# Kernel tuning notes

Measured on AMD Instinct MI355X. Metric: run time of the kernel, lower is better.

Reference implementation:

```python
import jax, jax.numpy as jnp
import numpy as np

IN_CH = 256
OUT_CH = 256
NUM_HEADS = 4
LOCAL_RADIUS = 2
SCALE = OUT_CH ** 0.5  # torch divides by out_channels**0.5


def setup_inputs() -> dict:
    key = jax.random.key(0)
    ks = jax.random.split(key, 7)
    B, C, H, W = 1, IN_CH, 48, 48
    x = jax.random.normal(ks[0], (B, C, H, W), dtype=jnp.float32)
    s = 0.02
    Wq = jax.random.normal(ks[1], (OUT_CH, IN_CH), dtype=jnp.float32) * s
    Wk = jax.random.normal(ks[2], (OUT_CH, IN_CH), dtype=jnp.float32) * s
    Wv = jax.random.normal(ks[3], (OUT_CH, IN_CH), dtype=jnp.float32) * s
    bq = jax.random.normal(ks[4], (OUT_CH,), dtype=jnp.float32) * s
    bk = jax.random.normal(ks[5], (OUT_CH,), dtype=jnp.float32) * s
    bv = jax.random.normal(ks[6], (OUT_CH,), dtype=jnp.float32) * s
    return {"x": x, "Wq": Wq, "bq": bq, "Wk": Wk, "bk": bk, "Wv": Wv, "bv": bv}


def reference(x, Wq, bq, Wk, bk, Wv, bv):
    B, C, H, W = x.shape
    N = H * W
    # Faithful to torch: x.view(B, N, -1) is a raw reshape of [B,C,H,W]
    xr = x.reshape(B, N, C)
    q = xr @ Wq.T + bq  # [B, N, OUT_CH]
    k = xr @ Wk.T + bk
    v = xr @ Wv.T + bv
    dh = OUT_CH // NUM_HEADS
    # [B, heads, N, dh]
    q = q.reshape(B, N, NUM_HEADS, dh).transpose(0, 2, 1, 3)
    k = k.reshape(B, N, NUM_HEADS, dh).transpose(0, 2, 1, 3)
    v = v.reshape(B, N, NUM_HEADS, dh).transpose(0, 2, 1, 3)
    acc = jnp.zeros_like(v)
    for h in range(-LOCAL_RADIUS, LOCAL_RADIUS + 1):
        for w in range(-LOCAL_RADIUS, LOCAL_RADIUS + 1):
            # torch rolls dims (-3, -2) of [B, heads, N, dh] -> axes (1, 2)
            rk = jnp.roll(k, shift=(h, w), axis=(1, 2))
            scores = jnp.einsum('bhnd,bhmd->bhnm', q, rk) / SCALE
            p = jax.nn.softmax(scores, axis=-1)  # dropout p=0 -> identity
            rv = jnp.roll(v, shift=(-h, -w), axis=(1, 2))
            acc = acc + jnp.einsum('bhnm,bhmd->bhnd', p, rv)
    out = acc.transpose(0, 2, 1, 3).reshape(B, N, NUM_HEADS * dh)
    return out
```

## Files before the change

kernel.cpp:

```cpp
#include <hip/hip_runtime.h>


#define N_TOK 2304
#define OUTC 256
#define HSZ (N_TOK * 64)

typedef _Float16 half8 __attribute__((ext_vector_type(8)));
typedef _Float16 half4 __attribute__((ext_vector_type(4)));
typedef float f32x4 __attribute__((ext_vector_type(4)));

__device__ __forceinline__ f32x4 mfma16(half8 a, half8 b, f32x4 c) {
  return __builtin_amdgcn_mfma_f32_16x16x32_f16(a, b, c, 0, 0, 0);
}

__global__ __launch_bounds__(256) void k_convert(
    const float* __restrict__ x, const float* __restrict__ Wq,
    const float* __restrict__ Wk, const float* __restrict__ Wv,
    _Float16* __restrict__ xh, _Float16* __restrict__ Wh) {
  int i = blockIdx.x * 256 + threadIdx.x;
  if (i < N_TOK * OUTC / 4) {
    float4 f = ((const float4*)x)[i];
    half4 h; h[0] = (_Float16)f.x; h[1] = (_Float16)f.y; h[2] = (_Float16)f.z; h[3] = (_Float16)f.w;
    ((half4*)xh)[i] = h;
  }
  if (i < OUTC * OUTC / 4) {
    float4 a = ((const float4*)Wq)[i];
    float4 b = ((const float4*)Wk)[i];
    float4 c = ((const float4*)Wv)[i];
    half4 ha, hb, hc;
    ha[0]=(_Float16)a.x; ha[1]=(_Float16)a.y; ha[2]=(_Float16)a.z; ha[3]=(_Float16)a.w;
    hb[0]=(_Float16)b.x; hb[1]=(_Float16)b.y; hb[2]=(_Float16)b.z; hb[3]=(_Float16)b.w;
    hc[0]=(_Float16)c.x; hc[1]=(_Float16)c.y; hc[2]=(_Float16)c.z; hc[3]=(_Float16)c.w;
    ((half4*)Wh)[i] = ha;
    ((half4*)(Wh + OUTC*OUTC))[i] = hb;
    ((half4*)(Wh + 2*OUTC*OUTC))[i] = hc;
  }
}

__global__ __launch_bounds__(256) void k_proj(
    const _Float16* __restrict__ xh, const _Float16* __restrict__ Wh,
    const float* __restrict__ bq, const float* __restrict__ bk,
    const float* __restrict__ bv,
    _Float16* __restrict__ Qh, _Float16* __restrict__ KF, float* __restrict__ VfT) {
  const int w = threadIdx.x >> 6, lane = threadIdx.x & 63;
  const int lr = lane & 15, lk = lane >> 4;
  const int n0 = blockIdx.x * 64 + w * 16;
  const int o0 = blockIdx.y * 64;
  const int mat = blockIdx.z;
  const _Float16* W = Wh + mat * (OUTC * OUTC);
  f32x4 acc[4] = {};
  const _Float16* xrow = xh + (n0 + lr) * OUTC + 8 * lk;
#pragma unroll
  for (int kk = 0; kk < 8; ++kk) {
    half8 a = *(const half8*)(xrow + 32 * kk);
#pragma unroll
    for (int c = 0; c < 4; ++c) {
      half8 b = *(const half8*)(W + (o0 + 16*c + lr) * OUTC + 32*kk + 8*lk);
      acc[c] = mfma16(a, b, acc[c]);
    }
  }
  const float* bias = (mat == 0) ? bq : (mat == 1) ? bk : bv;
  const int hd = blockIdx.y;
#pragma unroll
  for (int c = 0; c < 4; ++c) {
    int o = o0 + 16*c + lr;
    float bo = bias[o];
    if (mat == 2) {
      float4 vv;
      vv.x = acc[c][0] + bo; vv.y = acc[c][1] + bo;
      vv.z = acc[c][2] + bo; vv.w = acc[c][3] + bo;
      *(float4*)(VfT + (size_t)o * N_TOK + n0 + 4*lk) = vv;
    } else if (mat == 0) {
      int d = 16*c + lr;
#pragma unroll
      for (int r = 0; r < 4; ++r) {
        int n = n0 + 4*lk + r;
        Qh[((size_t)hd * N_TOK + n) * 64 + d] = (_Float16)((acc[c][r] + bo) * 0.0625f);
      }
    } else {
      int d = 16*c + lr;
      int h = d >> 5, g4K = (d >> 3) & 3, iiK = d & 7;
#pragma unroll
      for (int r = 0; r < 4; ++r) {
        int n = n0 + 4*lk + r;
        int tK = n >> 6, cK = (n >> 4) & 3, lrK = n & 15;
        KF[(size_t)hd * HSZ + ((tK*4 + cK)*2 + h)*512 + (g4K*16 + lrK)*8 + iiK] =
            (_Float16)(acc[c][r] + bo);
      }
    }
  }
}

__global__ __launch_bounds__(256) void k_smooth(
    const float* __restrict__ VfT, _Float16* __restrict__ VF) {
  const int t = blockIdx.x, vh = blockIdx.y;
  for (int f = threadIdx.x; f < 512; f += 256) {
    int cc = f >> 7, h = (f >> 6) & 1, g4 = (f >> 4) & 3, lr = f & 15;
    const float* src = VfT + (size_t)(vh*64 + 16*cc + lr) * N_TOK;
    int jbase = t*64 + 32*h + 4*g4;
    half8 out;
#pragma unroll
    for (int i = 0; i < 8; ++i) {
      int j = jbase + 16*(i >> 2) + (i & 3);
      float s = 0.f;
#pragma unroll
      for (int w = -4; w <= 4; w += 2) s += src[(j + w + N_TOK) % N_TOK];
      out[i] = (_Float16)s;
    }
    *(half8*)(VF + (size_t)vh * HSZ + (size_t)t * 4096 + f * 8) = out;
  }
}

__global__ __launch_bounds__(256) void k_flash(
    const _Float16* __restrict__ Qh, const _Float16* __restrict__ KF,
    const _Float16* __restrict__ VF, _Float16* __restrict__ Opart) {
  __shared__ __align__(16) float Lacc[4][32][68];
  __shared__ float Lsum[4][32];
  const int wv = threadIdx.x >> 6, lane = threadIdx.x & 63;
  const int lr = lane & 15, g4 = lane >> 4;
  const int n0 = blockIdx.x * 32;
  const int pair = blockIdx.y;
  const int hd = pair >> 2, gk = pair & 3;
  const int vh = (2*hd + 4 - gk) & 3;

  const _Float16* Qp = Qh + ((size_t)hd * N_TOK + n0 + lr) * 64 + 8*g4;
  const half8 qa0 = *(const half8*)(Qp);
  const half8 qa1 = *(const half8*)(Qp + 32);
  const half8 qb0 = *(const half8*)(Qp + 16*64);
  const half8 qb1 = *(const half8*)(Qp + 16*64 + 32);
  const _Float16* Kb = KF + (size_t)gk * HSZ + lane * 8;
  const _Float16* Vb = VF + (size_t)vh * HSZ + lane * 8;

  f32x4 accA[4] = {}, accB[4] = {};
  float lA = 0.f, lB = 0.f;

  auto loadT = [&](int t, half8 (&k)[8], half8 (&v)[8]) {
#pragma unroll
    for (int c = 0; c < 4; ++c) {
      const _Float16* pk = Kb + (size_t)t*4096 + c*1024;
      k[2*c]   = *(const half8*)(pk);
      k[2*c+1] = *(const half8*)(pk + 512);
      const _Float16* pv = Vb + (size_t)t*4096 + c*1024;
      v[2*c]   = *(const half8*)(pv);
      v[2*c+1] = *(const half8*)(pv + 512);
    }
  };
  auto body = [&](const half8 (&k)[8], const half8 (&v)[8],
                  half8 q0, half8 q1, f32x4 (&acc)[4], float& l_run) {
    f32x4 s[4];
    __builtin_amdgcn_s_setprio(1);
#pragma unroll
    for (int c = 0; c < 4; ++c) {
      f32x4 t = {};
      t = mfma16(k[2*c], q0, t);
      t = mfma16(k[2*c+1], q1, t);
      s[c] = t;
    }
    __builtin_amdgcn_s_setprio(0);
    float p[16], ps = 0.f;
#pragma unroll
    for (int c = 0; c < 4; ++c)
#pragma unroll
      for (int r = 0; r < 4; ++r) {
        float e = __expf(s[c][r]);
        p[4*c + r] = e;
        ps += e;
      }
    l_run += ps;
    half8 pb0, pb1;
#pragma unroll
    for (int ii = 0; ii < 8; ++ii) { pb0[ii] = (_Float16)p[ii]; pb1[ii] = (_Float16)p[8 + ii]; }
    __builtin_amdgcn_s_setprio(1);
#pragma unroll
    for (int cc = 0; cc < 4; ++cc) {
      acc[cc] = mfma16(v[2*cc], pb0, acc[cc]);
      acc[cc] = mfma16(v[2*cc+1], pb1, acc[cc]);
    }
    __builtin_amdgcn_s_setprio(0);
  };

  const int jt0 = wv * 9;
  half8 kA[8], vA[8], kB[8], vB[8];
  loadT(jt0, kA, vA);
#pragma unroll 1
  for (int u = 0; u < 4; ++u) {
    loadT(jt0 + 2*u + 1, kB, vB);
    body(kA, vA, qa0, qa1, accA, lA);
    body(kA, vA, qb0, qb1, accB, lB);
    loadT(jt0 + 2*u + 2, kA, vA);
    body(kB, vB, qa0, qa1, accA, lA);
    body(kB, vB, qb0, qb1, accB, lB);
  }
  body(kA, vA, qa0, qa1, accA, lA);
  body(kA, vA, qb0, qb1, accB, lB);

  lA += __shfl_xor(lA, 16); lA += __shfl_xor(lA, 32);
  lB += __shfl_xor(lB, 16); lB += __shfl_xor(lB, 32);

#pragma unroll
  for (int cc = 0; cc < 4; ++cc) {
    *(f32x4*)&Lacc[wv][lr][16*cc + 4*g4]      = accA[cc];
    *(f32x4*)&Lacc[wv][16 + lr][16*cc + 4*g4] = accB[cc];
  }
  if (g4 == 0) { Lsum[wv][lr] = lA; Lsum[wv][16 + lr] = lB; }
  __syncthreads();

  const int q = threadIdx.x >> 3, db = (threadIdx.x & 7) * 8;
  float lt = Lsum[0][q] + Lsum[1][q] + Lsum[2][q] + Lsum[3][q];
  float inv = 1.0f / lt;
  half8 o;
#pragma unroll
  for (int i = 0; i < 8; ++i) {
    float s = Lacc[0][q][db+i] + Lacc[1][q][db+i] + Lacc[2][q][db+i] + Lacc[3][q][db+i];
    o[i] = (_Float16)(s * inv);
  }
  *(half8*)(Opart + ((size_t)pair * N_TOK + n0 + q) * 64 + db) = o;
}

__global__ __launch_bounds__(256) void k_combine(
    const _Float16* __restrict__ Op, float* __restrict__ out) {
  int gid = blockIdx.x * 256 + threadIdx.x;
  int hd = gid / (N_TOK * 8);
  int rem = gid % (N_TOK * 8);
  int n = rem >> 3, db = (rem & 7) * 8;
  float acc[8] = {};
#pragma unroll
  for (int gk = 0; gk < 4; ++gk) {
    float cg = (((hd - gk) & 3) == 2) ? 2.0f : 1.0f;
    half8 v = *(const half8*)(Op + ((size_t)(hd*4 + gk) * N_TOK + n) * 64 + db);
#pragma unroll
    for (int i = 0; i < 8; ++i) acc[i] += cg * (float)v[i];
  }
  float* dst = out + (size_t)n * OUTC + hd * 64 + db;
  float4 r0, r1;
  r0.x = acc[0]; r0.y = acc[1]; r0.z = acc[2]; r0.w = acc[3];
  r1.x = acc[4]; r1.y = acc[5]; r1.z = acc[6]; r1.w = acc[7];
  *(float4*)(dst)     = r0;
  *(float4*)(dst + 4) = r1;
}

extern "C" void kernel_launch(void* const* d_in, const int* in_sizes, int n_in,
                              void* d_out, int out_size, void* d_ws, size_t ws_size,
                              hipStream_t stream) {
  (void)in_sizes; (void)n_in; (void)out_size; (void)ws_size;
  const float* x  = (const float*)d_in[0];
  const float* Wq = (const float*)d_in[1];
  const float* bq = (const float*)d_in[2];
  const float* Wk = (const float*)d_in[3];
  const float* bk = (const float*)d_in[4];
  const float* Wv = (const float*)d_in[5];
  const float* bv = (const float*)d_in[6];

  char* ws = (char*)d_ws;
  _Float16* xh  = (_Float16*)(ws);
  _Float16* Wh  = (_Float16*)(ws + 1179648);
  _Float16* Qh  = (_Float16*)(ws + 1572864);
  _Float16* KF  = (_Float16*)(ws + 2752512);
  float*    VfT = (float*)   (ws + 3932160);
  _Float16* VF  = (_Float16*)(ws + 6291456);
  _Float16* Op  = (_Float16*)(ws + 7471104);
  float* out = (float*)d_out;

  k_convert<<<dim3(576), dim3(256), 0, stream>>>(x, Wq, Wk, Wv, xh, Wh);
  k_proj   <<<dim3(36, 4, 3), dim3(256), 0, stream>>>(xh, Wh, bq, bk, bv, Qh, KF, VfT);
  k_smooth <<<dim3(36, 4), dim3(256), 0, stream>>>(VfT, VF);
  k_flash  <<<dim3(72, 16), dim3(256), 0, stream>>>(Qh, KF, VF, Op);
  k_combine<<<dim3(288), dim3(256), 0, stream>>>(Op, out);
}
```

Before: 82.68 us.

## Restructure flash attention: LDS-staged K/V tiles shared across waves, split-key chunks

Rewrites the attention kernel so that each block stages K and V tiles into double-buffered LDS through direct global-to-LDS loads. All four waves, each owning its own 16-query strip, then share those tiles. Previously each wave loaded its own tiles into registers. The key range is split into four chunks across a new grid dimension, so there are more blocks. Partial outputs and row sums go to workspace, and the combine kernel merges them with sum-weighted rescaling. Row sums are now computed with an MFMA against a ones vector, and exp is replaced by exp2 with log2(e) folded into the Q scale. The trade-off is extra partial-output traffic and a heavier combine step, plus a __syncthreads in every tile iteration.

```diff
diff --git a/kernel.cpp b/kernel.cpp
--- a/kernel.cpp
+++ b/kernel.cpp
@@ -9,8 +9,15 @@
 typedef _Float16 half4 __attribute__((ext_vector_type(4)));
 typedef float f32x4 __attribute__((ext_vector_type(4)));
 
+typedef __attribute__((address_space(3))) unsigned int as3_u32;
+typedef __attribute__((address_space(1))) unsigned int as1_u32;
+
 __device__ __forceinline__ f32x4 mfma16(half8 a, half8 b, f32x4 c) {
   return __builtin_amdgcn_mfma_f32_16x16x32_f16(a, b, c, 0, 0, 0);
+}
+
+__device__ __forceinline__ void gload_lds16(const _Float16* g, _Float16* l) {
+  __builtin_amdgcn_global_load_lds((const as1_u32*)g, (as3_u32*)l, 16, 0, 0);
 }
 
 __global__ __launch_bounds__(256) void k_convert(
@@ -72,10 +79,11 @@
       *(float4*)(VfT + (size_t)o * N_TOK + n0 + 4*lk) = vv;
     } else if (mat == 0) {
       int d = 16*c + lr;
+      const float qs = 0.0625f * 1.4426950408889634f;
 #pragma unroll
       for (int r = 0; r < 4; ++r) {
         int n = n0 + 4*lk + r;
-        Qh[((size_t)hd * N_TOK + n) * 64 + d] = (_Float16)((acc[c][r] + bo) * 0.0625f);
+        Qh[((size_t)hd * N_TOK + n) * 64 + d] = (_Float16)((acc[c][r] + bo) * qs);
       }
     } else {
       int d = 16*c + lr;
@@ -113,112 +121,98 @@
 
 __global__ __launch_bounds__(256) void k_flash(
     const _Float16* __restrict__ Qh, const _Float16* __restrict__ KF,
-    const _Float16* __restrict__ VF, _Float16* __restrict__ Opart) {
-  __shared__ __align__(16) float Lacc[4][32][68];
-  __shared__ float Lsum[4][32];
+    const _Float16* __restrict__ VF,
+    _Float16* __restrict__ Opart, float* __restrict__ Lpart) {
+  __shared__ __align__(16) _Float16 lds[2][8192];
   const int wv = threadIdx.x >> 6, lane = threadIdx.x & 63;
   const int lr = lane & 15, g4 = lane >> 4;
-  const int n0 = blockIdx.x * 32;
+  const int strip = blockIdx.x * 4 + wv;
+  const int n0 = strip * 16;
   const int pair = blockIdx.y;
   const int hd = pair >> 2, gk = pair & 3;
+  const int chunk = blockIdx.z;
   const int vh = (2*hd + 4 - gk) & 3;
 
   const _Float16* Qp = Qh + ((size_t)hd * N_TOK + n0 + lr) * 64 + 8*g4;
-  const half8 qa0 = *(const half8*)(Qp);
-  const half8 qa1 = *(const half8*)(Qp + 32);
-  const half8 qb0 = *(const half8*)(Qp + 16*64);
-  const half8 qb1 = *(const half8*)(Qp + 16*64 + 32);
-  const _Float16* Kb = KF + (size_t)gk * HSZ + lane * 8;
-  const _Float16* Vb = VF + (size_t)vh * HSZ + lane * 8;
-
-  f32x4 accA[4] = {}, accB[4] = {};
-  float lA = 0.f, lB = 0.f;
-
-  auto loadT = [&](int t, half8 (&k)[8], half8 (&v)[8]) {
-#pragma unroll
-    for (int c = 0; c < 4; ++c) {
-      const _Float16* pk = Kb + (size_t)t*4096 + c*1024;
-      k[2*c]   = *(const half8*)(pk);
-      k[2*c+1] = *(const half8*)(pk + 512);
-      const _Float16* pv = Vb + (size_t)t*4096 + c*1024;
-      v[2*c]   = *(const half8*)(pv);
-      v[2*c+1] = *(const half8*)(pv + 512);
-    }
+  const half8 q0 = *(const half8*)(Qp);
+  const half8 q1 = *(const half8*)(Qp + 32);
+
+  const _Float16* Kt = KF + (size_t)gk * HSZ + (size_t)chunk * 9 * 4096;
+  const _Float16* Vt = VF + (size_t)vh * HSZ + (size_t)chunk * 9 * 4096;
+  const _Float16* gsrc = (wv < 2 ? Kt : Vt) + (wv & 1) * 2048 + lane * 8;
+  const int ldsoff = (wv < 2 ? 0 : 4096) + (wv & 1) * 2048;
+
+  f32x4 acc[4] = {};
+  f32x4 accl = {};
+  half8 ones;
+#pragma unroll
+  for (int i = 0; i < 8; ++i) ones[i] = (_Float16)1.0f;
+
+  auto stage = [&](int t, int b) {
+    const _Float16* s = gsrc + (size_t)t * 4096;
+    _Float16* d = &lds[b][ldsoff];
+    gload_lds16(s,        d);
+    gload_lds16(s + 512,  d + 512);
+    gload_lds16(s + 1024, d + 1024);
+    gload_lds16(s + 1536, d + 1536);
   };
-  auto body = [&](const half8 (&k)[8], const half8 (&v)[8],
-                  half8 q0, half8 q1, f32x4 (&acc)[4], float& l_run) {
+  auto body = [&](int b) {
+    const _Float16* ldsK = &lds[b][0]    + lane * 8;
+    const _Float16* ldsV = &lds[b][4096] + lane * 8;
     f32x4 s[4];
     __builtin_amdgcn_s_setprio(1);
 #pragma unroll
     for (int c = 0; c < 4; ++c) {
       f32x4 t = {};
-      t = mfma16(k[2*c], q0, t);
-      t = mfma16(k[2*c+1], q1, t);
+      t = mfma16(*(const half8*)(ldsK + c*1024),       q0, t);
+      t = mfma16(*(const half8*)(ldsK + c*1024 + 512), q1, t);
       s[c] = t;
     }
     __builtin_amdgcn_s_setprio(0);
-    float p[16], ps = 0.f;
+    float p[16];
 #pragma unroll
     for (int c = 0; c < 4; ++c)
 #pragma unroll
-      for (int r = 0; r < 4; ++r) {
-        float e = __expf(s[c][r]);
-        p[4*c + r] = e;
-        ps += e;
-      }
-    l_run += ps;
+      for (int r = 0; r < 4; ++r) p[4*c + r] = exp2f(s[c][r]);
     half8 pb0, pb1;
 #pragma unroll
     for (int ii = 0; ii < 8; ++ii) { pb0[ii] = (_Float16)p[ii]; pb1[ii] = (_Float16)p[8 + ii]; }
     __builtin_amdgcn_s_setprio(1);
 #pragma unroll
     for (int cc = 0; cc < 4; ++cc) {
-      acc[cc] = mfma16(v[2*cc], pb0, acc[cc]);
-      acc[cc] = mfma16(v[2*cc+1], pb1, acc[cc]);
-    }
+      acc[cc] = mfma16(*(const half8*)(ldsV + cc*1024),       pb0, acc[cc]);
+      acc[cc] = mfma16(*(const half8*)(ldsV + cc*1024 + 512), pb1, acc[cc]);
+    }
+    accl = mfma16(ones, pb0, accl);
+    accl = mfma16(ones, pb1, accl);
     __builtin_amdgcn_s_setprio(0);
   };
 
-  const int jt0 = wv * 9;
-  half8 kA[8], vA[8], kB[8], vB[8];
-  loadT(jt0, kA, vA);
+  stage(0, 0);
+  __syncthreads();
 #pragma unroll 1
-  for (int u = 0; u < 4; ++u) {
-    loadT(jt0 + 2*u + 1, kB, vB);
-    body(kA, vA, qa0, qa1, accA, lA);
-    body(kA, vA, qb0, qb1, accB, lB);
-    loadT(jt0 + 2*u + 2, kA, vA);
-    body(kB, vB, qa0, qa1, accA, lA);
-    body(kB, vB, qb0, qb1, accB, lB);
-  }
-  body(kA, vA, qa0, qa1, accA, lA);
-  body(kA, vA, qb0, qb1, accB, lB);
-
-  lA += __shfl_xor(lA, 16); lA += __shfl_xor(lA, 32);
-  lB += __shfl_xor(lB, 16); lB += __shfl_xor(lB, 32);
-
+  for (int t = 0; t < 9; ++t) {
+    if (t < 8) stage(t + 1, (t + 1) & 1);
+    body(t & 1);
+    __syncthreads();
+  }
+
+  float inv = 1.0f / accl[0];
+  _Float16* Od = Opart + (((size_t)chunk * 16 + pair) * N_TOK + n0 + lr) * 64;
 #pragma unroll
   for (int cc = 0; cc < 4; ++cc) {
-    *(f32x4*)&Lacc[wv][lr][16*cc + 4*g4]      = accA[cc];
-    *(f32x4*)&Lacc[wv][16 + lr][16*cc + 4*g4] = accB[cc];
-  }
-  if (g4 == 0) { Lsum[wv][lr] = lA; Lsum[wv][16 + lr] = lB; }
-  __syncthreads();
-
-  const int q = threadIdx.x >> 3, db = (threadIdx.x & 7) * 8;
-  float lt = Lsum[0][q] + Lsum[1][q] + Lsum[2][q] + Lsum[3][q];
-  float inv = 1.0f / lt;
-  half8 o;
-#pragma unroll
-  for (int i = 0; i < 8; ++i) {
-    float s = Lacc[0][q][db+i] + Lacc[1][q][db+i] + Lacc[2][q][db+i] + Lacc[3][q][db+i];
-    o[i] = (_Float16)(s * inv);
-  }
-  *(half8*)(Opart + ((size_t)pair * N_TOK + n0 + q) * 64 + db) = o;
+    half4 h;
+#pragma unroll
+    for (int r = 0; r < 4; ++r) h[r] = (_Float16)(acc[cc][r] * inv);
+    *(half4*)(Od + 16*cc + 4*g4) = h;
+  }
+  if (g4 == 0)
+    Lpart[((size_t)chunk * 16 + pair) * N_TOK + n0 + lr] = accl[0];
 }
 
 __global__ __launch_bounds__(256) void k_combine(
-    const _Float16* __restrict__ Op, float* __restrict__ out) {
+    const _Float16* __restrict__ Opart, const float* __restrict__ Lpart,
+    float* __restrict__ out) {
   int gid = blockIdx.x * 256 + threadIdx.x;
   int hd = gid / (N_TOK * 8);
   int rem = gid % (N_TOK * 8);
@@ -227,9 +221,21 @@
 #pragma unroll
   for (int gk = 0; gk < 4; ++gk) {
     float cg = (((hd - gk) & 3) == 2) ? 2.0f : 1.0f;
-    half8 v = *(const half8*)(Op + ((size_t)(hd*4 + gk) * N_TOK + n) * 64 + db);
-#pragma unroll
-    for (int i = 0; i < 8; ++i) acc[i] += cg * (float)v[i];
+    int pair = hd * 4 + gk;
+    float la[4], lsum = 0.f;
+#pragma unroll
+    for (int ch = 0; ch < 4; ++ch) {
+      la[ch] = Lpart[((size_t)ch * 16 + pair) * N_TOK + n];
+      lsum += la[ch];
+    }
+    float rs = cg / lsum;
+#pragma unroll
+    for (int ch = 0; ch < 4; ++ch) {
+      half8 v = *(const half8*)(Opart + (((size_t)ch * 16 + pair) * N_TOK + n) * 64 + db);
+      float w = la[ch] * rs;
+#pragma unroll
+      for (int i = 0; i < 8; ++i) acc[i] += w * (float)v[i];
+    }
   }
   float* dst = out + (size_t)n * OUTC + hd * 64 + db;
   float4 r0, r1;
@@ -253,6 +259,7 @@
 
   char* ws = (char*)d_ws;
   _Float16* xh  = (_Float16*)(ws);
+  float*    Lp  = (float*)   (ws);
   _Float16* Wh  = (_Float16*)(ws + 1179648);
   _Float16* Qh  = (_Float16*)(ws + 1572864);
   _Float16* KF  = (_Float16*)(ws + 2752512);
@@ -264,6 +271,6 @@
   k_convert<<<dim3(576), dim3(256), 0, stream>>>(x, Wq, Wk, Wv, xh, Wh);
   k_proj   <<<dim3(36, 4, 3), dim3(256), 0, stream>>>(xh, Wh, bq, bk, bv, Qh, KF, VfT);
   k_smooth <<<dim3(36, 4), dim3(256), 0, stream>>>(VfT, VF);
-  k_flash  <<<dim3(72, 16), dim3(256), 0, stream>>>(Qh, KF, VF, Op);
-  k_combine<<<dim3(288), dim3(256), 0, stream>>>(Op, out);
-}
+  k_flash  <<<dim3(36, 16, 4), dim3(256), 0, stream>>>(Qh, KF, VF, Op, Lp);
+  k_combine<<<dim3(288), dim3(256), 0, stream>>>(Op, Lp, out);
+}
```

Result: faster. 73.97 us (-10.5%).
